# Kernel tuning notes

Measured on AMD Instinct MI355X. Metric: run time of the kernel, lower is better.

Reference implementation:

```python
import jax, jax.numpy as jnp
import numpy as np

N_NODES = 50000
N_REL = 1000
N_EDGES = 600000
D = 128
DEPTH = 2


def setup_inputs() -> dict:
    key = jax.random.key(0)
    ks = jax.random.split(key, 10)
    features = jax.random.normal(ks[0], (N_NODES, D), dtype=jnp.float32)
    rel_emb = jax.random.normal(ks[1], (N_REL, D), dtype=jnp.float32)
    # edge list: row0 = destination (sorted, matches coalesced sparse layout), row1 = source
    dst = jnp.sort(jax.random.randint(ks[2], (N_EDGES,), 0, N_NODES))
    src = jax.random.randint(ks[3], (N_EDGES,), 0, N_NODES)
    adj = jnp.stack([dst, src]).astype(jnp.int64)
    # one relation entry per triple: r_index[0]=triple id, r_index[1]=relation id
    r_index = jnp.stack([
        jnp.arange(N_EDGES, dtype=jnp.int64),
        jax.random.randint(ks[4], (N_EDGES,), 0, N_REL).astype(jnp.int64),
    ])
    r_val = jax.random.uniform(ks[5], (N_EDGES,), dtype=jnp.float32)
    # Xavier-ish params
    attn_w = jax.random.normal(ks[6], (3 * D, 1), dtype=jnp.float32) * 0.05
    attn_b = jnp.zeros((1,), dtype=jnp.float32)
    gate_w = jax.random.normal(ks[7], (3 * D, 1), dtype=jnp.float32) * 0.05
    gate_b = jnp.zeros((1,), dtype=jnp.float32)
    attn_kernels = jax.random.normal(ks[8], (DEPTH, D, 1), dtype=jnp.float32) * (6.0 / (D + 1)) ** 0.5
    return {"features": features, "rel_emb": rel_emb, "adj": adj, "r_index": r_index,
            "r_val": r_val, "attn_w": attn_w, "attn_b": attn_b, "gate_w": gate_w,
            "gate_b": gate_b, "attn_kernels": attn_kernels}


def _segment_softmax(vals, seg, n):
    # numerically stable softmax over edges grouped by destination node `seg`
    m = jax.ops.segment_max(vals, seg, num_segments=n)
    e = jnp.exp(vals - m[seg])
    s = jax.ops.segment_sum(e, seg, num_segments=n)
    return e / s[seg]


def reference(features, rel_emb, adj, r_index, r_val, attn_w, attn_b, gate_w, gate_b, attn_kernels):
    n_nodes = features.shape[0]
    n_triples = adj.shape[1]
    depth = attn_kernels.shape[0]
    dst, src_idx = adj[0], adj[1]

    feats = jnp.tanh(features)
    outs_c = [feats]
    outs_s = [feats]

    for l in range(depth):
        # sparse [triple, rel] @ rel_emb -> per-triple relation embedding
        tri_rel = jax.ops.segment_sum(r_val[:, None] * rel_emb[r_index[1]], r_index[0],
                                      num_segments=n_triples)  # [E, D]
        tri_rel = tri_rel / jnp.maximum(
            jnp.linalg.norm(tri_rel, axis=1, keepdims=True), 1e-12)
        # gather neighbors and reflect through relation hyperplane
        neighs = feats[src_idx]  # [E, D]
        neighs = neighs - 2.0 * jnp.sum(neighs * tri_rel, axis=1, keepdims=True) * tri_rel
        # structural attention + row-wise sparse softmax
        att_struct = _segment_softmax((tri_rel @ attn_kernels[l])[:, 0], dst, n_nodes)
        feats = jnp.tanh(jax.ops.segment_sum(neighs * att_struct[:, None], dst,
                                             num_segments=n_nodes))
        outs_c.append(feats)
        # semantic branch on updated features
        neighs2 = feats[src_idx]
        source_emb = feats[dst]
        diff_raw = source_emb - neighs2
        att_input = jnp.concatenate([source_emb, neighs2, diff_raw], axis=-1)  # [E, 3D]
        att_score = jnp.maximum(jax.nn.sigmoid(att_input @ attn_w + attn_b)[:, 0], 1e-4)
        gate_score = jax.nn.sigmoid(att_input @ gate_w + gate_b)[:, 0]
        final_att = gate_score * att_score + (1.0 - gate_score) * att_struct
        att = _segment_softmax(final_att, dst, n_nodes)
        new_diff = jnp.tanh(jax.ops.segment_sum(diff_raw * att[:, None], dst,
                                                num_segments=n_nodes))
        outs_s.append(new_diff)

    return (jnp.concatenate(outs_c, axis=-1), jnp.concatenate(outs_s, axis=-1))
```

## Files before the change

kernel.cpp:

```cpp
#include <hip/hip_runtime.h>
#include <math.h>

#define N_NODES 50000
#define N_REL   1000
#define N_EDGES 600000
#define D       128
#define OUT_COLS 384

#define FEAT0_BLOCKS  ((N_NODES * (D / 4) + 255) / 256)
#define RELN_BLOCKS   ((N_REL + 3) / 4)
#define ROWPTR_BLOCKS ((N_NODES + 1 + 255) / 256)
#define SETUP_BLOCKS  (FEAT0_BLOCKS + RELN_BLOCKS + ROWPTR_BLOCKS + 1)

__device__ __forceinline__ float wave_reduce_sum64(float v) {
#pragma unroll
    for (int m = 1; m < 64; m <<= 1) v += __shfl_xor(v, m, 64);
    return v;
}

__device__ __forceinline__ float group_reduce_sum16(float v) {
#pragma unroll
    for (int m = 1; m < 16; m <<= 1) v += __shfl_xor(v, m, 64);
    return v;
}

__device__ __forceinline__ float tanh_fast(float x) {
    float cx = fminf(fmaxf(x, -20.0f), 20.0f);
    float e = __expf(2.0f * cx);
    return __fdividef(e - 1.0f, e + 1.0f);
}

__device__ __forceinline__ float sigmoid_fast(float x) {
    return __fdividef(1.0f, 1.0f + __expf(-x));
}

__global__ __launch_bounds__(256) void k_setup(
        const float* __restrict__ features, const float* __restrict__ rel_emb,
        const float* __restrict__ attn_k, const float* __restrict__ attn_w,
        const float* __restrict__ gate_w, const int* __restrict__ dstv,
        float* __restrict__ out0, float* __restrict__ out1, float* __restrict__ fc0,
        float* __restrict__ rel_norm, float* __restrict__ er0, float* __restrict__ er1,
        float* __restrict__ wcomb, int* __restrict__ row_ptr) {
    int bid = blockIdx.x, tid = threadIdx.x;
    if (bid < FEAT0_BLOCKS) {
        int i = bid * 256 + tid;
        if (i >= N_NODES * (D / 4)) return;
        int n = i >> 5, q = i & 31;
        float4 f = *(const float4*)(features + (size_t)n * D + 4 * q);
        f.x = tanh_fast(f.x); f.y = tanh_fast(f.y);
        f.z = tanh_fast(f.z); f.w = tanh_fast(f.w);
        *(float4*)(out0 + (size_t)n * OUT_COLS + 4 * q) = f;
        *(float4*)(out1 + (size_t)n * OUT_COLS + 4 * q) = f;
        *(float4*)(fc0 + (size_t)n * D + 4 * q) = f;
    } else if (bid < FEAT0_BLOCKS + RELN_BLOCKS) {
        int wid  = (bid - FEAT0_BLOCKS) * 4 + (tid >> 6);
        int lane = tid & 63;
        if (wid >= N_REL) return;
        float2 v = *(const float2*)(rel_emb + (size_t)wid * D + 2 * lane);
        float sq = wave_reduce_sum64(v.x * v.x + v.y * v.y);
        float inv = 1.0f / fmaxf(sqrtf(sq), 1e-12f);
        float2 u = make_float2(v.x * inv, v.y * inv);
        *(float2*)(rel_norm + (size_t)wid * D + 2 * lane) = u;
        float2 k0 = *(const float2*)(attn_k + 2 * lane);
        float2 k1 = *(const float2*)(attn_k + D + 2 * lane);
        float d0 = wave_reduce_sum64(u.x * k0.x + u.y * k0.y);
        float d1 = wave_reduce_sum64(u.x * k1.x + u.y * k1.y);
        if (lane == 0) { er0[wid] = __expf(d0); er1[wid] = __expf(d1); }
    } else if (bid < FEAT0_BLOCKS + RELN_BLOCKS + ROWPTR_BLOCKS) {
        int n = (bid - FEAT0_BLOCKS - RELN_BLOCKS) * 256 + tid;
        if (n > N_NODES) return;
        int lo = 0, hi = N_EDGES;
        while (lo < hi) {
            int mid = (lo + hi) >> 1;
            if (dstv[mid] < n) lo = mid + 1; else hi = mid;
        }
        row_ptr[n] = lo;
    } else {
        int j = tid;
        if (j >= D) return;
        wcomb[j]         = attn_w[j] + attn_w[2 * D + j];
        wcomb[D + j]     = attn_w[D + j] - attn_w[2 * D + j];
        wcomb[2 * D + j] = gate_w[j] + gate_w[2 * D + j];
        wcomb[3 * D + j] = gate_w[D + j] - gate_w[2 * D + j];
    }
}

__global__ __launch_bounds__(256) void k_struct(
        const float* __restrict__ finC,
        float* __restrict__ foutC,
        float* __restrict__ foutS,
        const int* __restrict__ row_ptr, const int* __restrict__ srcv,
        const int* __restrict__ relv, const float* __restrict__ rval,
        const float* __restrict__ er,
        const float* __restrict__ rel_norm, const float* __restrict__ wcomb,
        float* __restrict__ node_Z, float* __restrict__ proj) {
    int n    = (blockIdx.x * blockDim.x + threadIdx.x) >> 6;
    int lane = threadIdx.x & 63;
    int g = lane >> 4, l = lane & 15;
    if (n >= N_NODES) return;
    int beg = row_ptr[n], end = row_ptr[n + 1];

    float4 acc0 = make_float4(0.f, 0.f, 0.f, 0.f);
    float4 acc1 = make_float4(0.f, 0.f, 0.f, 0.f);
    float Zp = 0.f;

    for (int cs = beg; cs < end; cs += 64) {
        int cnt = min(64, end - cs);
        int my_s = 0, my_r = -1; float my_w = 0.f;
        if (lane < cnt) {
            int e = cs + lane;
            my_s = srcv[e];
            int rr = relv[e];
            bool pos = rval[e] > 0.0f;
            my_r = pos ? rr : -1;
            my_w = pos ? er[rr] : 1.0f;
            Zp += my_w;
        }
        int nit = (cnt + 3) >> 2;
        for (int i = 0; i < nit; ++i) {
            int sl = (i << 2) | g;
            int   s = __shfl(my_s, sl, 64);
            int   r = __shfl(my_r, sl, 64);
            float w = __shfl(my_w, sl, 64);
            const float* xp = finC + (size_t)s * D + 8 * l;
            float4 x0 = *(const float4*)xp;
            float4 x1 = *(const float4*)(xp + 4);
            int rr = r < 0 ? 0 : r;
            const float* up = rel_norm + (size_t)rr * D + 8 * l;
            float4 u0 = *(const float4*)up;
            float4 u1 = *(const float4*)(up + 4);
            float p = x0.x*u0.x + x0.y*u0.y + x0.z*u0.z + x0.w*u0.w
                    + x1.x*u1.x + x1.y*u1.y + x1.z*u1.z + x1.w*u1.w;
            p = group_reduce_sum16(p);
            float wc = (r >= 0) ? 2.0f * w * p : 0.0f;
            acc0.x += w * x0.x - wc * u0.x;
            acc0.y += w * x0.y - wc * u0.y;
            acc0.z += w * x0.z - wc * u0.z;
            acc0.w += w * x0.w - wc * u0.w;
            acc1.x += w * x1.x - wc * u1.x;
            acc1.y += w * x1.y - wc * u1.y;
            acc1.z += w * x1.z - wc * u1.z;
            acc1.w += w * x1.w - wc * u1.w;
        }
    }
    float Z = wave_reduce_sum64(Zp);
#pragma unroll
    for (int m = 16; m < 64; m <<= 1) {
        acc0.x += __shfl_xor(acc0.x, m, 64);
        acc0.y += __shfl_xor(acc0.y, m, 64);
        acc0.z += __shfl_xor(acc0.z, m, 64);
        acc0.w += __shfl_xor(acc0.w, m, 64);
        acc1.x += __shfl_xor(acc1.x, m, 64);
        acc1.y += __shfl_xor(acc1.y, m, 64);
        acc1.z += __shfl_xor(acc1.z, m, 64);
        acc1.w += __shfl_xor(acc1.w, m, 64);
    }
    float invZ = (end > beg) ? (1.0f / Z) : 0.0f;
    float4 o0, o1;
    o0.x = tanh_fast(acc0.x * invZ); o0.y = tanh_fast(acc0.y * invZ);
    o0.z = tanh_fast(acc0.z * invZ); o0.w = tanh_fast(acc0.w * invZ);
    o1.x = tanh_fast(acc1.x * invZ); o1.y = tanh_fast(acc1.y * invZ);
    o1.z = tanh_fast(acc1.z * invZ); o1.w = tanh_fast(acc1.w * invZ);

    float pr[4];
#pragma unroll
    for (int k = 0; k < 4; ++k) {
        const float* wp = wcomb + k * D + 8 * l;
        float4 w0 = *(const float4*)wp;
        float4 w1 = *(const float4*)(wp + 4);
        float p = o0.x*w0.x + o0.y*w0.y + o0.z*w0.z + o0.w*w0.w
                + o1.x*w1.x + o1.y*w1.y + o1.z*w1.z + o1.w*w1.w;
        pr[k] = group_reduce_sum16(p);
    }
    if (lane == 0) {
        node_Z[n] = Z;
        *(float4*)(proj + 4 * (size_t)n) = make_float4(pr[0], pr[1], pr[2], pr[3]);
    }
    if (g == 0) {
        float* op = foutS + (size_t)n * OUT_COLS + 8 * l;
        *(float4*)op = o0;
        *(float4*)(op + 4) = o1;
        float* cp = foutC + (size_t)n * D + 8 * l;
        *(float4*)cp = o0;
        *(float4*)(cp + 4) = o1;
    }
}

__global__ __launch_bounds__(256) void k_sem(
        const float* __restrict__ featsC,
        float* __restrict__ oput,
        const int* __restrict__ row_ptr, const int* __restrict__ srcv,
        const int* __restrict__ relv, const float* __restrict__ rval,
        const float* __restrict__ er, const float* __restrict__ node_Z,
        const float* __restrict__ proj,
        const float* __restrict__ attn_b, const float* __restrict__ gate_b) {
    int n    = (blockIdx.x * blockDim.x + threadIdx.x) >> 6;
    int lane = threadIdx.x & 63;
    int g = lane >> 4, l = lane & 15;
    if (n >= N_NODES) return;
    int beg = row_ptr[n], end = row_ptr[n + 1];

    float4 pn = *(const float4*)(proj + 4 * (size_t)n);
    float ca = pn.x + attn_b[0];
    float cg = pn.z + gate_b[0];
    float invZ = (end > beg) ? (1.0f / node_Z[n]) : 0.0f;

    float4 acc0 = make_float4(0.f, 0.f, 0.f, 0.f);
    float4 acc1 = make_float4(0.f, 0.f, 0.f, 0.f);
    float Zs = 0.f;

    for (int cs = beg; cs < end; cs += 64) {
        int cnt = min(64, end - cs);
        int my_s = 0; float my_wt = 0.f;
        if (lane < cnt) {
            int e = cs + lane;
            my_s = srcv[e];
            int rr = relv[e];
            bool pos = rval[e] > 0.0f;
            float sw = (pos ? er[rr] : 1.0f) * invZ;
            float4 ps = *(const float4*)(proj + 4 * (size_t)my_s);
            float as = fmaxf(sigmoid_fast(ca + ps.y), 1e-4f);
            float gt = sigmoid_fast(cg + ps.w);
            my_wt = __expf(gt * as + (1.0f - gt) * sw);
            Zs += my_wt;
        }
        int nit = (cnt + 3) >> 2;
        for (int i = 0; i < nit; ++i) {
            int sl = (i << 2) | g;
            int   s  = __shfl(my_s, sl, 64);
            float wt = __shfl(my_wt, sl, 64);
            const float* xp = featsC + (size_t)s * D + 8 * l;
            float4 x0 = *(const float4*)xp;
            float4 x1 = *(const float4*)(xp + 4);
            acc0.x += wt * x0.x; acc0.y += wt * x0.y;
            acc0.z += wt * x0.z; acc0.w += wt * x0.w;
            acc1.x += wt * x1.x; acc1.y += wt * x1.y;
            acc1.z += wt * x1.z; acc1.w += wt * x1.w;
        }
    }
    Zs = wave_reduce_sum64(Zs);
#pragma unroll
    for (int m = 16; m < 64; m <<= 1) {
        acc0.x += __shfl_xor(acc0.x, m, 64);
        acc0.y += __shfl_xor(acc0.y, m, 64);
        acc0.z += __shfl_xor(acc0.z, m, 64);
        acc0.w += __shfl_xor(acc0.w, m, 64);
        acc1.x += __shfl_xor(acc1.x, m, 64);
        acc1.y += __shfl_xor(acc1.y, m, 64);
        acc1.z += __shfl_xor(acc1.z, m, 64);
        acc1.w += __shfl_xor(acc1.w, m, 64);
    }
    if (g == 0) {
        float invZs = (end > beg) ? (1.0f / Zs) : 0.0f;
        float sc    = (end > beg) ? 1.0f : 0.0f;
        const float* sp = featsC + (size_t)n * D + 8 * l;
        float4 s0 = *(const float4*)sp;
        float4 s1 = *(const float4*)(sp + 4);
        float4 o0, o1;
        o0.x = tanh_fast(sc * (s0.x - acc0.x * invZs));
        o0.y = tanh_fast(sc * (s0.y - acc0.y * invZs));
        o0.z = tanh_fast(sc * (s0.z - acc0.z * invZs));
        o0.w = tanh_fast(sc * (s0.w - acc0.w * invZs));
        o1.x = tanh_fast(sc * (s1.x - acc1.x * invZs));
        o1.y = tanh_fast(sc * (s1.y - acc1.y * invZs));
        o1.z = tanh_fast(sc * (s1.z - acc1.z * invZs));
        o1.w = tanh_fast(sc * (s1.w - acc1.w * invZs));
        float* op = oput + (size_t)n * OUT_COLS + 8 * l;
        *(float4*)op = o0;
        *(float4*)(op + 4) = o1;
    }
}

extern "C" void kernel_launch(void* const* d_in, const int* in_sizes, int n_in,
                              void* d_out, int out_size, void* d_ws, size_t ws_size,
                              hipStream_t stream) {
    const float* features = (const float*)d_in[0];
    const float* rel_emb  = (const float*)d_in[1];
    const int*   adj      = (const int*)d_in[2];
    const int*   r_index  = (const int*)d_in[3];
    const float* r_val    = (const float*)d_in[4];
    const float* attn_w   = (const float*)d_in[5];
    const float* attn_b   = (const float*)d_in[6];
    const float* gate_w   = (const float*)d_in[7];
    const float* gate_b   = (const float*)d_in[8];
    const float* attn_k   = (const float*)d_in[9];

    float* out0 = (float*)d_out;
    float* out1 = out0 + (size_t)N_NODES * OUT_COLS;

    float* rel_norm = (float*)d_ws;
    float* er0      = rel_norm + (size_t)N_REL * D;
    float* er1      = er0 + N_REL;
    float* wcomb    = er1 + N_REL;
    float* proj     = wcomb + 4 * D;
    float* node_Z   = proj + 4 * (size_t)N_NODES;
    int*   row_ptr  = (int*)(node_Z + N_NODES);
    float* fc0      = (float*)(row_ptr + N_NODES + 4);
    float* fc1      = fc0 + (size_t)N_NODES * D;
    float* fc2      = fc1 + (size_t)N_NODES * D;

    const int* dstv = adj;
    const int* srcv = adj + N_EDGES;
    const int* relv = r_index + N_EDGES;

    k_setup<<<SETUP_BLOCKS, 256, 0, stream>>>(
        features, rel_emb, attn_k, attn_w, gate_w, dstv,
        out0, out1, fc0, rel_norm, er0, er1, wcomb, row_ptr);

    const float* fcin[3] = {fc0, fc1, fc2};
    for (int l = 0; l < 2; ++l) {
        const float* er = l ? er1 : er0;
        k_struct<<<(N_NODES + 3) / 4, 256, 0, stream>>>(
            fcin[l], (float*)fcin[l + 1], out0 + (size_t)(l + 1) * D,
            row_ptr, srcv, relv, r_val, er, rel_norm, wcomb, node_Z, proj);
        k_sem<<<(N_NODES + 3) / 4, 256, 0, stream>>>(
            fcin[l + 1], out1 + (size_t)(l + 1) * D,
            row_ptr, srcv, relv, r_val, er, node_Z, proj, attn_b, gate_b);
    }
}
```

Baseline: 445.2 us.

## Store intermediate node features as bf16 and prefetch gathers across iterations

```diff
diff --git a/kernel.cpp b/kernel.cpp
--- a/kernel.cpp
+++ b/kernel.cpp
@@ -7,6 +7,8 @@
 #define D       128
 #define OUT_COLS 384
 
+typedef unsigned short ushortT;
+
 #define FEAT0_BLOCKS  ((N_NODES * (D / 4) + 255) / 256)
 #define RELN_BLOCKS   ((N_REL + 3) / 4)
 #define ROWPTR_BLOCKS ((N_NODES + 1 + 255) / 256)
@@ -18,9 +20,16 @@
     return v;
 }
 
-__device__ __forceinline__ float group_reduce_sum16(float v) {
-#pragma unroll
-    for (int m = 1; m < 16; m <<= 1) v += __shfl_xor(v, m, 64);
+template <int CTRL>
+__device__ __forceinline__ float dpp_add_(float v) {
+    int t = __builtin_amdgcn_update_dpp(0, __float_as_int(v), CTRL, 0xf, 0xf, true);
+    return v + __int_as_float(t);
+}
+__device__ __forceinline__ float group_sum16(float v) {
+    v = dpp_add_<0xB1>(v);
+    v = dpp_add_<0x4E>(v);
+    v = dpp_add_<0x141>(v);
+    v = dpp_add_<0x140>(v);
     return v;
 }
 
@@ -29,16 +38,32 @@
     float e = __expf(2.0f * cx);
     return __fdividef(e - 1.0f, e + 1.0f);
 }
-
 __device__ __forceinline__ float sigmoid_fast(float x) {
     return __fdividef(1.0f, 1.0f + __expf(-x));
+}
+
+__device__ __forceinline__ void bf16x8_to_f32(uint4 q, float4& a, float4& b) {
+    a.x = __int_as_float((int)(q.x << 16));
+    a.y = __int_as_float((int)(q.x & 0xffff0000u));
+    a.z = __int_as_float((int)(q.y << 16));
+    a.w = __int_as_float((int)(q.y & 0xffff0000u));
+    b.x = __int_as_float((int)(q.z << 16));
+    b.y = __int_as_float((int)(q.z & 0xffff0000u));
+    b.z = __int_as_float((int)(q.w << 16));
+    b.w = __int_as_float((int)(q.w & 0xffff0000u));
+}
+__device__ __forceinline__ unsigned pack_bf16x2(float lo, float hi) {
+    unsigned a = __float_as_uint(lo), b = __float_as_uint(hi);
+    a = (a + 0x7fffu + ((a >> 16) & 1u)) >> 16;
+    b = (b + 0x7fffu + ((b >> 16) & 1u));
+    return (a & 0xffffu) | (b & 0xffff0000u);
 }
 
 __global__ __launch_bounds__(256) void k_setup(
         const float* __restrict__ features, const float* __restrict__ rel_emb,
         const float* __restrict__ attn_k, const float* __restrict__ attn_w,
         const float* __restrict__ gate_w, const int* __restrict__ dstv,
-        float* __restrict__ out0, float* __restrict__ out1, float* __restrict__ fc0,
+        float* __restrict__ out0, float* __restrict__ out1, ushortT* __restrict__ fc0,
         float* __restrict__ rel_norm, float* __restrict__ er0, float* __restrict__ er1,
         float* __restrict__ wcomb, int* __restrict__ row_ptr) {
     int bid = blockIdx.x, tid = threadIdx.x;
@@ -51,7 +76,8 @@
         f.z = tanh_fast(f.z); f.w = tanh_fast(f.w);
         *(float4*)(out0 + (size_t)n * OUT_COLS + 4 * q) = f;
         *(float4*)(out1 + (size_t)n * OUT_COLS + 4 * q) = f;
-        *(float4*)(fc0 + (size_t)n * D + 4 * q) = f;
+        uint2 p = make_uint2(pack_bf16x2(f.x, f.y), pack_bf16x2(f.z, f.w));
+        *((uint2*)(fc0 + (size_t)n * D) + q) = p;
     } else if (bid < FEAT0_BLOCKS + RELN_BLOCKS) {
         int wid  = (bid - FEAT0_BLOCKS) * 4 + (tid >> 6);
         int lane = tid & 63;
@@ -86,8 +112,8 @@
 }
 
 __global__ __launch_bounds__(256) void k_struct(
-        const float* __restrict__ finC,
-        float* __restrict__ foutC,
+        const ushortT* __restrict__ finC,
+        ushortT* __restrict__ foutC,
         float* __restrict__ foutS,
         const int* __restrict__ row_ptr, const int* __restrict__ srcv,
         const int* __restrict__ relv, const float* __restrict__ rval,
@@ -117,33 +143,50 @@
             Zp += my_w;
         }
         int nit = (cnt + 3) >> 2;
-        for (int i = 0; i < nit; ++i) {
-            int sl = (i << 2) | g;
-            int   s = __shfl(my_s, sl, 64);
-            int   r = __shfl(my_r, sl, 64);
-            float w = __shfl(my_w, sl, 64);
-            const float* xp = finC + (size_t)s * D + 8 * l;
-            float4 x0 = *(const float4*)xp;
-            float4 x1 = *(const float4*)(xp + 4);
+        int   s = __shfl(my_s, g, 64);
+        int   r = __shfl(my_r, g, 64);
+        float w = __shfl(my_w, g, 64);
+        uint4 xq = *((const uint4*)(finC + (size_t)s * D) + l);
+        {
             int rr = r < 0 ? 0 : r;
             const float* up = rel_norm + (size_t)rr * D + 8 * l;
             float4 u0 = *(const float4*)up;
             float4 u1 = *(const float4*)(up + 4);
-            float p = x0.x*u0.x + x0.y*u0.y + x0.z*u0.z + x0.w*u0.w
-                    + x1.x*u1.x + x1.y*u1.y + x1.z*u1.z + x1.w*u1.w;
-            p = group_reduce_sum16(p);
-            float wc = (r >= 0) ? 2.0f * w * p : 0.0f;
-            acc0.x += w * x0.x - wc * u0.x;
-            acc0.y += w * x0.y - wc * u0.y;
-            acc0.z += w * x0.z - wc * u0.z;
-            acc0.w += w * x0.w - wc * u0.w;
-            acc1.x += w * x1.x - wc * u1.x;
-            acc1.y += w * x1.y - wc * u1.y;
-            acc1.z += w * x1.z - wc * u1.z;
-            acc1.w += w * x1.w - wc * u1.w;
-        }
-    }
-    float Z = wave_reduce_sum64(Zp);
+            for (int i = 0; i < nit; ++i) {
+                int s_c = s; int r_c = r; float w_c = w;
+                uint4 xq_c = xq; float4 u0_c = u0, u1_c = u1;
+                (void)s_c;
+                if (i + 1 < nit) {
+                    int sl2 = ((i + 1) << 2) | g;
+                    s = __shfl(my_s, sl2, 64);
+                    r = __shfl(my_r, sl2, 64);
+                    w = __shfl(my_w, sl2, 64);
+                    xq = *((const uint4*)(finC + (size_t)s * D) + l);
+                    int rr2 = r < 0 ? 0 : r;
+                    const float* up2 = rel_norm + (size_t)rr2 * D + 8 * l;
+                    u0 = *(const float4*)up2;
+                    u1 = *(const float4*)(up2 + 4);
+                }
+                float4 x0, x1;
+                bf16x8_to_f32(xq_c, x0, x1);
+                float p = x0.x*u0_c.x + x0.y*u0_c.y + x0.z*u0_c.z + x0.w*u0_c.w
+                        + x1.x*u1_c.x + x1.y*u1_c.y + x1.z*u1_c.z + x1.w*u1_c.w;
+                p = group_sum16(p);
+                float wc = (r_c >= 0) ? 2.0f * w_c * p : 0.0f;
+                acc0.x += w_c * x0.x - wc * u0_c.x;
+                acc0.y += w_c * x0.y - wc * u0_c.y;
+                acc0.z += w_c * x0.z - wc * u0_c.z;
+                acc0.w += w_c * x0.w - wc * u0_c.w;
+                acc1.x += w_c * x1.x - wc * u1_c.x;
+                acc1.y += w_c * x1.y - wc * u1_c.y;
+                acc1.z += w_c * x1.z - wc * u1_c.z;
+                acc1.w += w_c * x1.w - wc * u1_c.w;
+            }
+        }
+    }
+    float Z = group_sum16(Zp);
+    Z += __shfl_xor(Z, 16, 64);
+    Z += __shfl_xor(Z, 32, 64);
 #pragma unroll
     for (int m = 16; m < 64; m <<= 1) {
         acc0.x += __shfl_xor(acc0.x, m, 64);
@@ -170,7 +213,7 @@
         float4 w1 = *(const float4*)(wp + 4);
         float p = o0.x*w0.x + o0.y*w0.y + o0.z*w0.z + o0.w*w0.w
                 + o1.x*w1.x + o1.y*w1.y + o1.z*w1.z + o1.w*w1.w;
-        pr[k] = group_reduce_sum16(p);
+        pr[k] = group_sum16(p);
     }
     if (lane == 0) {
         node_Z[n] = Z;
@@ -180,14 +223,15 @@
         float* op = foutS + (size_t)n * OUT_COLS + 8 * l;
         *(float4*)op = o0;
         *(float4*)(op + 4) = o1;
-        float* cp = foutC + (size_t)n * D + 8 * l;
-        *(float4*)cp = o0;
-        *(float4*)(cp + 4) = o1;
+        uint4 pk = make_uint4(pack_bf16x2(o0.x, o0.y), pack_bf16x2(o0.z, o0.w),
+                              pack_bf16x2(o1.x, o1.y), pack_bf16x2(o1.z, o1.w));
+        *((uint4*)(foutC + (size_t)n * D) + l) = pk;
     }
 }
 
 __global__ __launch_bounds__(256) void k_sem(
-        const float* __restrict__ featsC,
+        const ushortT* __restrict__ featsC,
+        const float* __restrict__ seF,
         float* __restrict__ oput,
         const int* __restrict__ row_ptr, const int* __restrict__ srcv,
         const int* __restrict__ relv, const float* __restrict__ rval,
@@ -225,20 +269,28 @@
             Zs += my_wt;
         }
         int nit = (cnt + 3) >> 2;
+        int   s  = __shfl(my_s, g, 64);
+        float wt = __shfl(my_wt, g, 64);
+        uint4 xq = *((const uint4*)(featsC + (size_t)s * D) + l);
         for (int i = 0; i < nit; ++i) {
-            int sl = (i << 2) | g;
-            int   s  = __shfl(my_s, sl, 64);
-            float wt = __shfl(my_wt, sl, 64);
-            const float* xp = featsC + (size_t)s * D + 8 * l;
-            float4 x0 = *(const float4*)xp;
-            float4 x1 = *(const float4*)(xp + 4);
-            acc0.x += wt * x0.x; acc0.y += wt * x0.y;
-            acc0.z += wt * x0.z; acc0.w += wt * x0.w;
-            acc1.x += wt * x1.x; acc1.y += wt * x1.y;
-            acc1.z += wt * x1.z; acc1.w += wt * x1.w;
-        }
-    }
-    Zs = wave_reduce_sum64(Zs);
+            float wt_c = wt; uint4 xq_c = xq;
+            if (i + 1 < nit) {
+                int sl2 = ((i + 1) << 2) | g;
+                s  = __shfl(my_s, sl2, 64);
+                wt = __shfl(my_wt, sl2, 64);
+                xq = *((const uint4*)(featsC + (size_t)s * D) + l);
+            }
+            float4 x0, x1;
+            bf16x8_to_f32(xq_c, x0, x1);
+            acc0.x += wt_c * x0.x; acc0.y += wt_c * x0.y;
+            acc0.z += wt_c * x0.z; acc0.w += wt_c * x0.w;
+            acc1.x += wt_c * x1.x; acc1.y += wt_c * x1.y;
+            acc1.z += wt_c * x1.z; acc1.w += wt_c * x1.w;
+        }
+    }
+    Zs = group_sum16(Zs);
+    Zs += __shfl_xor(Zs, 16, 64);
+    Zs += __shfl_xor(Zs, 32, 64);
 #pragma unroll
     for (int m = 16; m < 64; m <<= 1) {
         acc0.x += __shfl_xor(acc0.x, m, 64);
@@ -253,7 +305,7 @@
     if (g == 0) {
         float invZs = (end > beg) ? (1.0f / Zs) : 0.0f;
         float sc    = (end > beg) ? 1.0f : 0.0f;
-        const float* sp = featsC + (size_t)n * D + 8 * l;
+        const float* sp = seF + (size_t)n * OUT_COLS + 8 * l;
         float4 s0 = *(const float4*)sp;
         float4 s1 = *(const float4*)(sp + 4);
         float4 o0, o1;
@@ -295,9 +347,9 @@
     float* proj     = wcomb + 4 * D;
     float* node_Z   = proj + 4 * (size_t)N_NODES;
     int*   row_ptr  = (int*)(node_Z + N_NODES);
-    float* fc0      = (float*)(row_ptr + N_NODES + 4);
-    float* fc1      = fc0 + (size_t)N_NODES * D;
-    float* fc2      = fc1 + (size_t)N_NODES * D;
+    ushortT* fc0    = (ushortT*)(row_ptr + N_NODES + 4);
+    ushortT* fc1    = fc0 + (size_t)N_NODES * D;
+    ushortT* fc2    = fc1 + (size_t)N_NODES * D;
 
     const int* dstv = adj;
     const int* srcv = adj + N_EDGES;
@@ -307,14 +359,14 @@
         features, rel_emb, attn_k, attn_w, gate_w, dstv,
         out0, out1, fc0, rel_norm, er0, er1, wcomb, row_ptr);
 
-    const float* fcin[3] = {fc0, fc1, fc2};
+    const ushortT* fcin[3] = {fc0, fc1, fc2};
     for (int l = 0; l < 2; ++l) {
         const float* er = l ? er1 : er0;
         k_struct<<<(N_NODES + 3) / 4, 256, 0, stream>>>(
-            fcin[l], (float*)fcin[l + 1], out0 + (size_t)(l + 1) * D,
+            fcin[l], (ushortT*)fcin[l + 1], out0 + (size_t)(l + 1) * D,
             row_ptr, srcv, relv, r_val, er, rel_norm, wcomb, node_Z, proj);
         k_sem<<<(N_NODES + 3) / 4, 256, 0, stream>>>(
-            fcin[l + 1], out1 + (size_t)(l + 1) * D,
+            fcin[l + 1], out0 + (size_t)(l + 1) * D, out1 + (size_t)(l + 1) * D,
             row_ptr, srcv, relv, r_val, er, node_Z, proj, attn_b, gate_b);
     }
 }
```

After: 376.9 us. -15.3%, faster.
